# Optimization experiments

Measured on AMD Instinct MI355X. Metric: run time of the kernel, lower is better.

## Reference

```python
import jax, jax.numpy as jnp
import numpy as np

# Static module configuration (from init_kwargs)
BL, BS = 256, 256            # batch_size_large, batch_size_small
R_LARGE, R_SMALL = 64, 16
R_MULT = R_LARGE // R_SMALL  # 4: each large adapter split into 4 rank-16 slices
D = 4096
N_SPLIT = 32 * R_MULT + 64   # 192 splitted adapters
LB = BL * R_MULT + BS        # 1280 lora rows


def setup_inputs() -> dict:
    key = jax.random.key(0)
    k1, k2, k3, k4, k5 = jax.random.split(key, 5)
    x = jax.random.normal(k1, (BL + BS, 1, D), dtype=jnp.float16)
    lora_A = jax.random.normal(k2, (N_SPLIT, D, R_SMALL), dtype=jnp.float16) * jnp.float16(0.02)
    lora_B = jax.random.normal(k3, (N_SPLIT, R_SMALL, D), dtype=jnp.float16) * jnp.float16(0.02)
    xids = jax.random.randint(k4, (LB,), 0, BL + BS, dtype=jnp.int32)
    wids = jax.random.randint(k5, (LB,), 0, N_SPLIT, dtype=jnp.int32)
    return {"x": x, "lora_A": lora_A, "lora_B": lora_B, "xids": xids, "wids": wids}


def reference(x, lora_A, lora_B, xids, wids):
    # gather token activations and per-row rank-16 adapter slices
    xg = x[xids]                 # [LB, 1, D]
    Ag = lora_A[wids]            # [LB, D, r]
    Bg = lora_B[wids]            # [LB, r, D]
    h = jnp.einsum('bod,bdr->bor', xg, Ag)          # [LB, 1, r]
    y = jnp.einsum('bor,brd->bod', h, Bg) * jnp.float16(2.0)  # [LB, 1, D]
    # split+sum: first BL groups of R_MULT rows are summed (keepdims),
    # last BS rows pass through -> equivalent to a segment-sum.
    seg = jnp.concatenate([jnp.repeat(jnp.arange(BL), R_MULT), BL + jnp.arange(BS)])
    z = jax.ops.segment_sum(y[:, 0, :], seg, num_segments=BL + BS)  # [BL+BS, D]
    return z[:, None, :]         # [batch_size, 1, D]
```

## Files before the change

### kernel.cpp

```cpp
#include <hip/hip_runtime.h>
#include <stdint.h>

typedef __attribute__((ext_vector_type(4))) float float4v;

#define D 4096
#define R 16
#define NW 192
#define LB 1280
#define NBL 256
#define MAXB 32
#define NWAVE 16

__global__ __launch_bounds__(1024) void fused_kernel(
    const float* __restrict__ x,
    const float* __restrict__ A,
    const float* __restrict__ B,
    const int* __restrict__ xids,
    const int* __restrict__ wids,
    float* __restrict__ ybuf,
    float* __restrict__ out)
{
    const int w = blockIdx.x;
    const int t = threadIdx.x;
    const int lane = t & 63;
    const int wave = t >> 6;

    __shared__ int list[MAXB];
    __shared__ int xidl[MAXB];
    __shared__ int cnt;
    __shared__ float hws[MAXB][NWAVE][17];
    __shared__ float hl[MAXB][R];

    if (t == 0) cnt = 0;
    __syncthreads();
    for (int i = t; i < LB; i += 1024)
        if (wids[i] == w) { int q = atomicAdd(&cnt, 1); if (q < MAXB) list[q] = i; }
    __syncthreads();
    int n = cnt > MAXB ? MAXB : cnt;
    if (n == 0) return;
    if (t < n) xidl[t] = xids[list[t]];
    __syncthreads();

    const float4v* af = (const float4v*)(A + (size_t)w * D * R);
    float4v a[16];
    #pragma unroll
    for (int k = 0; k < 16; ++k) a[k] = af[1024 * wave + 64 * k + lane];

    const int dof = 256 * wave + (lane >> 2);
    for (int i = 0; i < n; ++i) {
        const float* xr = x + (size_t)xidl[i] * D + dof;
        float h0 = 0.f, h1 = 0.f, h2 = 0.f, h3 = 0.f;
        #pragma unroll
        for (int k = 0; k < 16; ++k) {
            const float xd = xr[16 * k];
            h0 += xd * a[k][0];
            h1 += xd * a[k][1];
            h2 += xd * a[k][2];
            h3 += xd * a[k][3];
        }
        #pragma unroll
        for (int off = 4; off <= 32; off <<= 1) {
            h0 += __shfl_xor(h0, off, 64);
            h1 += __shfl_xor(h1, off, 64);
            h2 += __shfl_xor(h2, off, 64);
            h3 += __shfl_xor(h3, off, 64);
        }
        if (lane < 4) {
            hws[i][wave][4 * lane + 0] = h0;
            hws[i][wave][4 * lane + 1] = h1;
            hws[i][wave][4 * lane + 2] = h2;
            hws[i][wave][4 * lane + 3] = h3;
        }
    }
    __syncthreads();
    for (int idx = t; idx < n * R; idx += 1024) {
        const int i = idx >> 4, r = idx & 15;
        float s = 0.f;
        #pragma unroll
        for (int j = 0; j < NWAVE; ++j) s += hws[i][j][r];
        hl[i][r] = s;
    }
    __syncthreads();

    const float* Bw = B + (size_t)w * R * D + 4 * t;
    float4v breg[R];
    #pragma unroll
    for (int r = 0; r < R; ++r) breg[r] = *(const float4v*)(Bw + (size_t)r * D);

    for (int i = 0; i < n; ++i) {
        const int b = list[i];
        float4v acc = {0.f, 0.f, 0.f, 0.f};
        #pragma unroll
        for (int r = 0; r < R; ++r) {
            const float hr = hl[i][r];
            acc[0] += hr * breg[r][0];
            acc[1] += hr * breg[r][1];
            acc[2] += hr * breg[r][2];
            acc[3] += hr * breg[r][3];
        }
        #pragma unroll
        for (int k = 0; k < 4; ++k) acc[k] *= 2.0f;

        if (b < NBL * 4) {
            *(float4v*)(ybuf + (size_t)b * D + 4 * t) = acc;
        } else {
            *(float4v*)(out + (size_t)(NBL + (b - NBL * 4)) * D + 4 * t) = acc;
        }
    }
}

__global__ __launch_bounds__(256) void sum4_kernel(
    const float* __restrict__ ybuf,
    float* __restrict__ out)
{
    const int o = blockIdx.x >> 2;
    const int q = blockIdx.x & 3;
    const int col = q * 1024 + 4 * threadIdx.x;
    const float* y0 = ybuf + (size_t)(4 * o) * D + col;
    float4v v0 = *(const float4v*)(y0);
    float4v v1 = *(const float4v*)(y0 + D);
    float4v v2 = *(const float4v*)(y0 + 2 * D);
    float4v v3 = *(const float4v*)(y0 + 3 * D);
    float4v s;
    #pragma unroll
    for (int k = 0; k < 4; ++k) s[k] = (v0[k] + v1[k]) + (v2[k] + v3[k]);
    *(float4v*)(out + (size_t)o * D + col) = s;
}

extern "C" void kernel_launch(void* const* d_in, const int* in_sizes, int n_in,
                              void* d_out, int out_size, void* d_ws, size_t ws_size,
                              hipStream_t stream) {
    const float* x    = (const float*)d_in[0];
    const float* A    = (const float*)d_in[1];
    const float* B    = (const float*)d_in[2];
    const int*   xids = (const int*)d_in[3];
    const int*   wids = (const int*)d_in[4];
    float*       out  = (float*)d_out;

    float* ybuf = (float*)d_ws;

    hipLaunchKernelGGL(fused_kernel, dim3(NW), dim3(1024), 0, stream,
                       x, A, B, xids, wids, ybuf, out);
    hipLaunchKernelGGL(sum4_kernel, dim3(NBL * 4), dim3(256), 0, stream,
                       ybuf, out);
}
```

Before: 153.4 us.

## Split fused LoRA kernel into D-chunked h and y kernels with more blocks

Replaces the single 192-block, 1024-thread fused kernel with two kernels of 768 blocks of 256 threads each. Each block handles one quarter of D. The h kernel writes partial rank-16 projections into a scratch region of the output buffer, and the y kernel sums the four partials before applying B. The h kernel also stages x rows through shared memory and prefetches the next row to hide load latency. The aim is better occupancy across CUs, at the cost of an extra launch, repeating the wids scan in both kernels, and a global round-trip for h.

Result: no change. 152.6 us (-0.5%).

```diff
diff --git a/kernel.cpp b/kernel.cpp
--- a/kernel.cpp
+++ b/kernel.cpp
@@ -9,83 +9,118 @@
 #define LB 1280
 #define NBL 256
 #define MAXB 32
-#define NWAVE 16
 
-__global__ __launch_bounds__(1024) void fused_kernel(
+
+__global__ __launch_bounds__(256) void h_kernel(
     const float* __restrict__ x,
     const float* __restrict__ A,
-    const float* __restrict__ B,
     const int* __restrict__ xids,
     const int* __restrict__ wids,
-    float* __restrict__ ybuf,
-    float* __restrict__ out)
+    float* __restrict__ hp)
 {
-    const int w = blockIdx.x;
+    const int w = blockIdx.x >> 2;
+    const int c = blockIdx.x & 3;
     const int t = threadIdx.x;
     const int lane = t & 63;
-    const int wave = t >> 6;
+    const int wv = t >> 6;
 
     __shared__ int list[MAXB];
     __shared__ int xidl[MAXB];
     __shared__ int cnt;
-    __shared__ float hws[MAXB][NWAVE][17];
+    __shared__ float hws[MAXB][4][17];
+    __shared__ float xs[4][256];
+
+    if (t == 0) cnt = 0;
+    __syncthreads();
+    for (int i = t; i < LB; i += 256)
+        if (wids[i] == w) { int q = atomicAdd(&cnt, 1); if (q < MAXB) list[q] = i; }
+    __syncthreads();
+    const int n = cnt > MAXB ? MAXB : cnt;
+    if (n == 0) return;
+    if (t < n) xidl[t] = xids[list[t]];
+    __syncthreads();
+
+    const int xoff = 1024 * c + 256 * wv + 4 * lane;
+
+    float4v xv = *(const float4v*)(x + (size_t)xidl[0] * D + xoff);
+
+    const float4v* af = (const float4v*)(A + ((size_t)w * D + 1024 * c) * R);
+    float4v a[16];
+    #pragma unroll
+    for (int k = 0; k < 16; ++k) a[k] = af[1024 * wv + 64 * k + lane];
+
+    *(float4v*)(&xs[wv][4 * lane]) = xv;
+    for (int i = 0; i < n; ++i) {
+        float4v xvn;
+        if (i + 1 < n)
+            xvn = *(const float4v*)(x + (size_t)xidl[i + 1] * D + xoff);
+        float h0 = 0.f, h1 = 0.f, h2 = 0.f, h3 = 0.f;
+        #pragma unroll
+        for (int k = 0; k < 16; ++k) {
+            const float xd = xs[wv][(lane >> 2) + 16 * k];
+            h0 += xd * a[k][0]; h1 += xd * a[k][1];
+            h2 += xd * a[k][2]; h3 += xd * a[k][3];
+        }
+        #pragma unroll
+        for (int off = 4; off <= 32; off <<= 1) {
+            h0 += __shfl_xor(h0, off, 64); h1 += __shfl_xor(h1, off, 64);
+            h2 += __shfl_xor(h2, off, 64); h3 += __shfl_xor(h3, off, 64);
+        }
+        if (lane < 4) {
+            hws[i][wv][4 * lane + 0] = h0;
+            hws[i][wv][4 * lane + 1] = h1;
+            hws[i][wv][4 * lane + 2] = h2;
+            hws[i][wv][4 * lane + 3] = h3;
+        }
+        if (i + 1 < n)
+            *(float4v*)(&xs[wv][4 * lane]) = xvn;
+    }
+    __syncthreads();
+
+    for (int idx = t; idx < n * R; idx += 256) {
+        const int i = idx >> 4, r = idx & 15;
+        const float s = hws[i][0][r] + hws[i][1][r] + hws[i][2][r] + hws[i][3][r];
+        hp[((size_t)c * LB + list[i]) * R + r] = s;
+    }
+}
+
+__global__ __launch_bounds__(256) void y_kernel(
+    const float* __restrict__ B,
+    const int* __restrict__ wids,
+    float* __restrict__ ybuf,
+    float* out)
+{
+    const int w = blockIdx.x >> 2;
+    const int cq = blockIdx.x & 3;
+    const int t = threadIdx.x;
+
+    __shared__ int list[MAXB];
+    __shared__ int cnt;
     __shared__ float hl[MAXB][R];
 
     if (t == 0) cnt = 0;
     __syncthreads();
-    for (int i = t; i < LB; i += 1024)
+    for (int i = t; i < LB; i += 256)
         if (wids[i] == w) { int q = atomicAdd(&cnt, 1); if (q < MAXB) list[q] = i; }
     __syncthreads();
-    int n = cnt > MAXB ? MAXB : cnt;
+    const int n = cnt > MAXB ? MAXB : cnt;
     if (n == 0) return;
-    if (t < n) xidl[t] = xids[list[t]];
     __syncthreads();
 
-    const float4v* af = (const float4v*)(A + (size_t)w * D * R);
-    float4v a[16];
-    #pragma unroll
-    for (int k = 0; k < 16; ++k) a[k] = af[1024 * wave + 64 * k + lane];
-
-    const int dof = 256 * wave + (lane >> 2);
-    for (int i = 0; i < n; ++i) {
-        const float* xr = x + (size_t)xidl[i] * D + dof;
-        float h0 = 0.f, h1 = 0.f, h2 = 0.f, h3 = 0.f;
-        #pragma unroll
-        for (int k = 0; k < 16; ++k) {
-            const float xd = xr[16 * k];
-            h0 += xd * a[k][0];
-            h1 += xd * a[k][1];
-            h2 += xd * a[k][2];
-            h3 += xd * a[k][3];
-        }
-        #pragma unroll
-        for (int off = 4; off <= 32; off <<= 1) {
-            h0 += __shfl_xor(h0, off, 64);
-            h1 += __shfl_xor(h1, off, 64);
-            h2 += __shfl_xor(h2, off, 64);
-            h3 += __shfl_xor(h3, off, 64);
-        }
-        if (lane < 4) {
-            hws[i][wave][4 * lane + 0] = h0;
-            hws[i][wave][4 * lane + 1] = h1;
-            hws[i][wave][4 * lane + 2] = h2;
-            hws[i][wave][4 * lane + 3] = h3;
-        }
-    }
-    __syncthreads();
-    for (int idx = t; idx < n * R; idx += 1024) {
-        const int i = idx >> 4, r = idx & 15;
-        float s = 0.f;
-        #pragma unroll
-        for (int j = 0; j < NWAVE; ++j) s += hws[i][j][r];
-        hl[i][r] = s;
-    }
-    __syncthreads();
-
-    const float* Bw = B + (size_t)w * R * D + 4 * t;
+    const int col = 1024 * cq + 4 * t;
+    const float* Bw = B + (size_t)w * R * D + col;
     float4v breg[R];
     #pragma unroll
     for (int r = 0; r < R; ++r) breg[r] = *(const float4v*)(Bw + (size_t)r * D);
+
+    const float* hp = out;
+    for (int idx = t; idx < n * R; idx += 256) {
+        const int i = idx >> 4, r = idx & 15;
+        const size_t base = (size_t)list[i] * R + r;
+        hl[i][r] = hp[base] + hp[(size_t)LB * R + base]
+                 + hp[2 * (size_t)LB * R + base] + hp[3 * (size_t)LB * R + base];
+    }
+    __syncthreads();
 
     for (int i = 0; i < n; ++i) {
         const int b = list[i];
@@ -102,9 +137,9 @@
         for (int k = 0; k < 4; ++k) acc[k] *= 2.0f;
 
         if (b < NBL * 4) {
-            *(float4v*)(ybuf + (size_t)b * D + 4 * t) = acc;
+            *(float4v*)(ybuf + (size_t)b * D + col) = acc;
         } else {
-            *(float4v*)(out + (size_t)(NBL + (b - NBL * 4)) * D + 4 * t) = acc;
+            *(float4v*)(out + (size_t)(NBL + (b - NBL * 4)) * D + col) = acc;
         }
     }
 }
@@ -139,8 +174,10 @@
 
     float* ybuf = (float*)d_ws;
 
-    hipLaunchKernelGGL(fused_kernel, dim3(NW), dim3(1024), 0, stream,
-                       x, A, B, xids, wids, ybuf, out);
+    hipLaunchKernelGGL(h_kernel, dim3(NW * 4), dim3(256), 0, stream,
+                       x, A, xids, wids, out);
+    hipLaunchKernelGGL(y_kernel, dim3(NW * 4), dim3(256), 0, stream,
+                       B, wids, ybuf, out);
     hipLaunchKernelGGL(sum4_kernel, dim3(NBL * 4), dim3(256), 0, stream,
                        ybuf, out);
 }
```
